# Kernel optimization log

Measured on AMD Instinct MI355X. Metric: run time of the kernel, lower is better.

Reference implementation:

```python
import jax, jax.numpy as jnp
import numpy as np

# ---- module constants (from init_kwargs) ----
EMBED_DIM = 384
NUM_HYPEREDGES = 128
TOPK = 64
SPATIAL_SHAPE = (16, 32, 32)  # D, H, W -> N = 16384
SPACING = (2.0, 1.0, 1.0)
SPATIAL_WEIGHT = 0.1
B, N, C = 4, 16 * 32 * 32, EMBED_DIM


def _l2norm(x, axis=-1, eps=1e-12):
    n = jnp.linalg.norm(x, axis=axis, keepdims=True)
    return x / jnp.maximum(n, eps)


def _get_3d_coords():
    D, H, W = SPATIAL_SHAPE
    z = jnp.arange(D, dtype=jnp.float32) * SPACING[0]
    y = jnp.arange(H, dtype=jnp.float32) * SPACING[1]
    x = jnp.arange(W, dtype=jnp.float32) * SPACING[2]
    zz, yy, xx = jnp.meshgrid(z, y, x, indexing='ij')
    return jnp.stack([zz, yy, xx], axis=-1).reshape(-1, 3)  # (N, 3)


def setup_inputs() -> dict:
    key = jax.random.key(0)
    k1, k2 = jax.random.split(key)
    node_features = jax.random.normal(k1, (B, N, C), dtype=jnp.float32)
    class_token = jax.random.normal(k2, (1, 1, C), dtype=jnp.float32)
    temperature = jnp.ones((1,), dtype=jnp.float32) * 0.07
    return {"node_features": node_features, "class_token": class_token, "temperature": temperature}


def reference(node_features, class_token, temperature):
    Ne = NUM_HYPEREDGES
    w = SPATIAL_WEIGHT
    temp = temperature[0]

    nodes_n = _l2norm(node_features)                      # (B, N, C)

    # Step 1: center sampling by semantic similarity to class token
    ct_n = _l2norm(jnp.broadcast_to(class_token, (B, 1, C)))
    scores = jnp.einsum('boc,bnc->bn', ct_n, nodes_n) / temp  # (B, N)
    _, center_idx = jax.lax.top_k(scores, Ne)             # (B, Ne)

    # Gather centers and compute cosine sim of every center vs all nodes
    centers = jnp.take_along_axis(node_features, center_idx[:, :, None], axis=1)  # (B, Ne, C)
    centers_n = _l2norm(centers)
    sem_sim = jnp.einsum('bec,bnc->ben', centers_n, nodes_n) / temp  # (B, Ne, N)

    # Spatial bias (normalized distance from each center voxel)
    coords = _get_3d_coords()                             # (N, 3)
    center_coords = coords[center_idx]                    # (B, Ne, 3)
    diff = coords[None, None, :, :] - center_coords[:, :, None, :]  # (B, Ne, N, 3)
    dist = jnp.linalg.norm(diff, axis=-1)                 # (B, Ne, N)
    dist = dist / (jnp.max(dist, axis=-1, keepdims=True) + 1e-8)
    combined = (1.0 - w) * sem_sim + w * (1.0 - dist)     # (B, Ne, N)

    # Per-hyperedge top-K neighbors -> incidence matrix H (B, N, Ne)
    _, nbr_idx = jax.lax.top_k(combined, TOPK)            # (B, Ne, K)
    b_ix = jnp.arange(B)[:, None, None]
    e_ix = jnp.arange(Ne)[None, :, None]
    Hmat = jnp.zeros((B, N, Ne), dtype=node_features.dtype)
    Hmat = Hmat.at[b_ix, nbr_idx, e_ix].set(1.0)
    return Hmat
```

## Files before the change

kernel.cpp:

```cpp
#include <hip/hip_runtime.h>
#include <math.h>

#define BB 4
#define NN 16384
#define CC 384
#define NE 128
#define KK 64
#define EQCAP 256

typedef unsigned short ushort_t;
typedef __attribute__((ext_vector_type(8))) short bf16x8;
typedef __attribute__((ext_vector_type(4))) float f32x4;
#define MFMA(a, b, c) __builtin_amdgcn_mfma_f32_16x16x32_bf16(a, b, c, 0, 0, 0)

__device__ inline unsigned fkey(float f) {
    unsigned b = __float_as_uint(f);
    return (b & 0x80000000u) ? ~b : (b | 0x80000000u);
}
__device__ inline ushort_t bf16rne(float f) {
    unsigned u = __float_as_uint(f);
    unsigned r = u + 0x7FFFu + ((u >> 16) & 1u);
    return (ushort_t)(r >> 16);
}
__device__ inline float bf16tof(ushort_t h) {
    return __uint_as_float(((unsigned)h) << 16);
}
__device__ inline void cvt2(float fa, float fb, unsigned& hp, unsigned& lp) {
    unsigned ua = __float_as_uint(fa), ub = __float_as_uint(fb);
    unsigned ra = ua + 0x8000u, rb = ub + 0x8000u;
    hp = (ra >> 16) | (rb & 0xFFFF0000u);
    float ha = __uint_as_float(ra & 0xFFFF0000u);
    float hb = __uint_as_float(rb & 0xFFFF0000u);
    float la = fa - ha, lb = fb - hb;
    unsigned lra = __float_as_uint(la) + 0x8000u;
    unsigned lrb = __float_as_uint(lb) + 0x8000u;
    lp = (lra >> 16) | (lrb & 0xFFFF0000u);
}
__device__ inline void gload16(const void* g, void* l) {
    __builtin_amdgcn_global_load_lds(
        (const __attribute__((address_space(1))) void*)g,
        (__attribute__((address_space(3))) void*)l, 16, 0, 0);
}

__device__ inline void bin_select(unsigned* hist, int t, int* wsum,
                                  int* sh_bin, int* sh_r, int r) {
    int lane = t & 63, wid = t >> 6;
    int c = (t < 256) ? (int)hist[t] : 0;
    int x = c;
#pragma unroll
    for (int off = 1; off < 64; off <<= 1) {
        int v = __shfl_down(x, off, 64);
        if (lane + off < 64) x += v;
    }
    if (lane == 0 && wid < 4) wsum[wid] = x;
    __syncthreads();
    if (t < 256) {
        int add = 0;
        for (int w2 = wid + 1; w2 < 4; ++w2) add += wsum[w2];
        int S_incl = x + add;
        int S_excl = S_incl - c;
        if (S_excl < r && S_incl >= r) { *sh_bin = t; *sh_r = r - S_excl; }
    }
    __syncthreads();
}

__global__ __launch_bounds__(256) void k_scores(const float* __restrict__ nf,
                                                const float* __restrict__ ct,
                                                unsigned* __restrict__ keys,
                                                float* __restrict__ invn) {
    int wave = threadIdx.x >> 6;
    int lane = threadIdx.x & 63;
    int row  = blockIdx.x * 4 + wave;
    const float* x = nf + (size_t)row * CC;
    float4 a  = ((const float4*)x)[lane];
    float2 c2 = ((const float2*)(x + 256))[lane];
    float4 ta = ((const float4*)ct)[lane];
    float2 tc = ((const float2*)(ct + 256))[lane];
    float ss = a.x*a.x + a.y*a.y + a.z*a.z + a.w*a.w + c2.x*c2.x + c2.y*c2.y;
    float dt = ta.x*a.x + ta.y*a.y + ta.z*a.z + ta.w*a.w + tc.x*c2.x + tc.y*c2.y;
#pragma unroll
    for (int off = 32; off; off >>= 1) {
        ss += __shfl_xor(ss, off, 64);
        dt += __shfl_xor(dt, off, 64);
    }
    if (lane == 0) {
        float inv = 1.0f / fmaxf(sqrtf(ss), 1e-12f);
        invn[row] = inv;
        keys[row] = fkey(dt * inv);
    }
}

__global__ __launch_bounds__(1024) void k_top128(const unsigned* __restrict__ keys,
                                                 const float* __restrict__ nf,
                                                 const float* __restrict__ invn,
                                                 ushort_t* __restrict__ Ahi,
                                                 ushort_t* __restrict__ Alo,
                                                 float* __restrict__ meta) {
    __shared__ unsigned hist[256];
    __shared__ int wsum[4];
    __shared__ int sh_bin, sh_r;
    __shared__ unsigned cu[NE];
    __shared__ int cil[NE];
    __shared__ int eqi[EQCAP];
    __shared__ int cnt_gt, cnt_eq;
    __shared__ int ocid[NE];
    int b = blockIdx.x;
    int t = threadIdx.x;
    const uint4* rowv = (const uint4*)(keys + b * NN);
    if (t == 0) { cnt_gt = 0; cnt_eq = 0; }
    unsigned prefix = 0;
    int r = NE;
#pragma unroll
    for (int pass = 0; pass < 4; ++pass) {
        int shift = 24 - 8 * pass;
        unsigned hm = (pass == 0) ? 0u : (0xFFFFFFFFu << (shift + 8));
        if (t < 256) hist[t] = 0;
        __syncthreads();
#pragma unroll
        for (int i = 0; i < 4; ++i) {
            uint4 u = rowv[t + 1024 * i];
            if ((u.x & hm) == (prefix & hm)) atomicAdd(&hist[(u.x >> shift) & 255], 1u);
            if ((u.y & hm) == (prefix & hm)) atomicAdd(&hist[(u.y >> shift) & 255], 1u);
            if ((u.z & hm) == (prefix & hm)) atomicAdd(&hist[(u.z >> shift) & 255], 1u);
            if ((u.w & hm) == (prefix & hm)) atomicAdd(&hist[(u.w >> shift) & 255], 1u);
        }
        __syncthreads();
        bin_select(hist, t, wsum, &sh_bin, &sh_r, r);
        prefix |= ((unsigned)sh_bin) << shift;
        r = sh_r;
        __syncthreads();
    }
    unsigned T = prefix;
#pragma unroll
    for (int i = 0; i < 4; ++i) {
        uint4 u = rowv[t + 1024 * i];
        int nb = 4 * (t + 1024 * i);
        unsigned vv[4] = {u.x, u.y, u.z, u.w};
#pragma unroll
        for (int cmp = 0; cmp < 4; ++cmp) {
            if (vv[cmp] > T) {
                int p = atomicAdd(&cnt_gt, 1);
                cu[p] = vv[cmp]; cil[p] = nb + cmp;
            } else if (vv[cmp] == T) {
                int p = atomicAdd(&cnt_eq, 1);
                if (p < EQCAP) eqi[p] = nb + cmp;
            }
        }
    }
    __syncthreads();
    int ne = cnt_eq < EQCAP ? cnt_eq : EQCAP;
    if (t < ne) {
        int mine = eqi[t], rk = 0;
        for (int j = 0; j < ne; ++j) rk += (eqi[j] < mine);
        if (rk < r) { int p = cnt_gt + rk; cu[p] = T; cil[p] = mine; }
    }
    __syncthreads();
    if (t < NE) {
        unsigned mu = cu[t]; int mi = cil[t], rk = 0;
#pragma unroll 4
        for (int j = 0; j < NE; ++j) {
            unsigned ou = cu[j]; int oi = cil[j];
            rk += (ou > mu) || (ou == mu && oi < mi);
        }
        ocid[rk] = mi;
    }
    __syncthreads();
    {
        int e = t >> 3, part = t & 7;
        int ci = ocid[e];
        float inv = invn[b * NN + ci];
        const float4* src = (const float4*)(nf + ((size_t)b * NN + ci) * CC) + part * 12;
        ushort_t* dh = Ahi + ((size_t)b * NE + e) * CC + part * 48;
        ushort_t* dl = Alo + ((size_t)b * NE + e) * CC + part * 48;
#pragma unroll
        for (int i = 0; i < 12; ++i) {
            float4 f = src[i];
            f.x *= inv; f.y *= inv; f.z *= inv; f.w *= inv;
            ushort4 h, l;
            h.x = bf16rne(f.x); l.x = bf16rne(f.x - bf16tof(h.x));
            h.y = bf16rne(f.y); l.y = bf16rne(f.y - bf16tof(h.y));
            h.z = bf16rne(f.z); l.z = bf16rne(f.z - bf16tof(h.z));
            h.w = bf16rne(f.w); l.w = bf16rne(f.w - bf16tof(h.w));
            ((ushort4*)dh)[i] = h;
            ((ushort4*)dl)[i] = l;
        }
    }
    if (t < NE) {
        int ci = ocid[t];
        float zc = (float)(ci >> 10) * 2.0f;
        float yc = (float)((ci >> 5) & 31);
        float xc = (float)(ci & 31);
        float mz = fmaxf(zc * zc, (30.f - zc) * (30.f - zc));
        float my = fmaxf(yc * yc, (31.f - yc) * (31.f - yc));
        float mx = fmaxf(xc * xc, (31.f - xc) * (31.f - xc));
        float md = sqrtf(mz + my + mx);
        int be = b * NE + t;
        meta[be * 4 + 0] = zc;
        meta[be * 4 + 1] = yc;
        meta[be * 4 + 2] = xc;
        meta[be * 4 + 3] = 1.0f / (md + 1e-8f);
    }
}

__global__ __launch_bounds__(256, 4) void k_gemm(const float* __restrict__ nf,
                                                 const ushort_t* __restrict__ Ahi,
                                                 const ushort_t* __restrict__ Alo,
                                                 const float* __restrict__ invn,
                                                 const float* __restrict__ meta,
                                                 const float* __restrict__ temp,
                                                 unsigned* __restrict__ outk) {
    __shared__ ushort_t Ah[4096], Al[4096];
    __shared__ ushort_t Bhs[2048], Bls[2048];
    __shared__ float ms[NE * 4];
    __shared__ float invs_s[64];
    int b  = blockIdx.y;
    int n0 = blockIdx.x * 64;
    int t  = threadIdx.x;
    int w = t >> 6, lane = t & 63, quad = lane >> 4, mrow = lane & 15;
    int m0 = (w & 1) * 64, nw0 = (w >> 1) * 32;
    for (int i = t; i < NE * 4; i += 256) ms[i] = meta[b * NE * 4 + i];
    if (t < 64) invs_s[t] = invn[b * NN + n0 + t];
    f32x4 acc[4][2];
#pragma unroll
    for (int i = 0; i < 4; ++i)
#pragma unroll
        for (int j = 0; j < 2; ++j) acc[i][j] = (f32x4)0.f;
    const ushort_t* Abh = Ahi + (size_t)b * NE * CC;
    const ushort_t* Abl = Alo + (size_t)b * NE * CC;
    const float* Bb = nf + ((size_t)b * NN + n0) * CC;
    int bn = t >> 2, bk8 = t & 3;
    const float* bsrc = Bb + (size_t)bn * CC + bk8 * 8;
    ushort_t* bh_dst = &Bhs[(bk8 * 64 + bn) * 8];
    ushort_t* bl_dst = &Bls[(bk8 * 64 + bn) * 8];
    const ushort_t* agh0 = Abh + (size_t)(w * 16 + mrow) * CC + quad * 8;
    const ushort_t* agh1 = Abh + (size_t)((w + 4) * 16 + mrow) * CC + quad * 8;
    const ushort_t* agl0 = Abl + (size_t)(w * 16 + mrow) * CC + quad * 8;
    const ushort_t* agl1 = Abl + (size_t)((w + 4) * 16 + mrow) * CC + quad * 8;
    for (int kt = 0; kt < CC; kt += 32) {
        __syncthreads();
        gload16(agh0 + kt, &Ah[w * 512]);
        gload16(agh1 + kt, &Ah[(w + 4) * 512]);
        gload16(agl0 + kt, &Al[w * 512]);
        gload16(agl1 + kt, &Al[(w + 4) * 512]);
        {
            const float4* bs = (const float4*)(bsrc + kt);
            float4 f0 = bs[0];
            float4 f1 = bs[1];
            uint4 ph, pl;
            cvt2(f0.x, f0.y, ph.x, pl.x);
            cvt2(f0.z, f0.w, ph.y, pl.y);
            cvt2(f1.x, f1.y, ph.z, pl.z);
            cvt2(f1.z, f1.w, ph.w, pl.w);
            *(uint4*)bh_dst = ph;
            *(uint4*)bl_dst = pl;
        }
        __syncthreads();
        bf16x8 afh[4], afl[4], bfh[2], bfl[2];
#pragma unroll
        for (int i = 0; i < 4; ++i) {
            int m = m0 + i * 16 + mrow;
            int off = (m >> 4) * 512 + quad * 128 + (m & 15) * 8;
            afh[i] = *(const bf16x8*)&Ah[off];
            afl[i] = *(const bf16x8*)&Al[off];
        }
#pragma unroll
        for (int j = 0; j < 2; ++j) {
            int n = nw0 + j * 16 + mrow;
            bfh[j] = *(const bf16x8*)&Bhs[(quad * 64 + n) * 8];
            bfl[j] = *(const bf16x8*)&Bls[(quad * 64 + n) * 8];
        }
#pragma unroll
        for (int i = 0; i < 4; ++i)
#pragma unroll
            for (int j = 0; j < 2; ++j) {
                acc[i][j] = MFMA(afh[i], bfh[j], acc[i][j]);
                acc[i][j] = MFMA(afh[i], bfl[j], acc[i][j]);
                acc[i][j] = MFMA(afl[i], bfh[j], acc[i][j]);
            }
    }
    float scale = 0.9f / temp[0];
#pragma unroll
    for (int j = 0; j < 2; ++j) {
        int nloc = nw0 + j * 16 + mrow;
        int n = n0 + nloc;
        float invnn = invs_s[nloc];
        float zf = (float)(n >> 10) * 2.0f;
        float yf = (float)((n >> 5) & 31);
        float xf = (float)(n & 31);
#pragma unroll
        for (int i = 0; i < 4; ++i) {
#pragma unroll
            for (int r = 0; r < 4; ++r) {
                int e = m0 + i * 16 + quad * 4 + r;
                float zc = ms[e * 4 + 0], yc = ms[e * 4 + 1], xc = ms[e * 4 + 2], ivd = ms[e * 4 + 3];
                float dz = zf - zc, dy = yf - yc, dx = xf - xc;
                float dist = sqrtf(dz * dz + dy * dy + dx * dx);
                float v = scale * invnn * acc[i][j][r] + 0.1f * (1.0f - dist * ivd);
                outk[((size_t)(b * NE + e)) * NN + n] = fkey(v);
            }
        }
    }
}

__global__ __launch_bounds__(1024) void k_top64(const unsigned* __restrict__ comb,
                                                int* __restrict__ sel) {
    __shared__ unsigned hist[256];
    __shared__ int wsum[4];
    __shared__ int sh_bin, sh_r;
    __shared__ int eqi[EQCAP];
    __shared__ int cnt_gt, cnt_eq;
    int be = blockIdx.x;
    int t  = threadIdx.x;
    const uint4* rowv = (const uint4*)(comb + (size_t)be * NN);
    if (t == 0) { cnt_gt = 0; cnt_eq = 0; }
    unsigned prefix = 0;
    int r = KK;
#pragma unroll
    for (int pass = 0; pass < 4; ++pass) {
        int shift = 24 - 8 * pass;
        unsigned hm = (pass == 0) ? 0u : (0xFFFFFFFFu << (shift + 8));
        if (t < 256) hist[t] = 0;
        __syncthreads();
#pragma unroll
        for (int i = 0; i < 4; ++i) {
            uint4 u = rowv[t + 1024 * i];
            if ((u.x & hm) == (prefix & hm)) atomicAdd(&hist[(u.x >> shift) & 255], 1u);
            if ((u.y & hm) == (prefix & hm)) atomicAdd(&hist[(u.y >> shift) & 255], 1u);
            if ((u.z & hm) == (prefix & hm)) atomicAdd(&hist[(u.z >> shift) & 255], 1u);
            if ((u.w & hm) == (prefix & hm)) atomicAdd(&hist[(u.w >> shift) & 255], 1u);
        }
        __syncthreads();
        bin_select(hist, t, wsum, &sh_bin, &sh_r, r);
        prefix |= ((unsigned)sh_bin) << shift;
        r = sh_r;
        __syncthreads();
    }
    unsigned T = prefix;
#pragma unroll
    for (int i = 0; i < 4; ++i) {
        uint4 u = rowv[t + 1024 * i];
        int nb = 4 * (t + 1024 * i);
        unsigned vv[4] = {u.x, u.y, u.z, u.w};
#pragma unroll
        for (int cmp = 0; cmp < 4; ++cmp) {
            if (vv[cmp] > T) {
                int p = atomicAdd(&cnt_gt, 1);
                sel[be * KK + p] = nb + cmp;
            } else if (vv[cmp] == T) {
                int p = atomicAdd(&cnt_eq, 1);
                if (p < EQCAP) eqi[p] = nb + cmp;
            }
        }
    }
    __syncthreads();
    int ne = cnt_eq < EQCAP ? cnt_eq : EQCAP;
    if (t < ne) {
        int mine = eqi[t], rk = 0;
        for (int j = 0; j < ne; ++j) rk += (eqi[j] < mine);
        if (rk < r) sel[be * KK + cnt_gt + rk] = mine;
    }
}

__global__ __launch_bounds__(256) void k_scatter(const int* __restrict__ sel,
                                                 float* __restrict__ H) {
    int gid = blockIdx.x * 256 + threadIdx.x;
    int b = gid >> 13;
    int e = (gid >> 6) & 127;
    int n = sel[gid];
    H[((size_t)b * NN + n) * NE + e] = 1.0f;
}

extern "C" void kernel_launch(void* const* d_in, const int* in_sizes, int n_in,
                              void* d_out, int out_size, void* d_ws, size_t ws_size,
                              hipStream_t stream) {
    const float* nf   = (const float*)d_in[0];
    const float* ct   = (const float*)d_in[1];
    const float* temp = (const float*)d_in[2];
    float* out = (float*)d_out;

    unsigned* keys = (unsigned*)d_ws;
    float* invn    = (float*)(keys + BB * NN);
    float* meta    = invn + BB * NN;
    ushort_t* Ahi  = (ushort_t*)(meta + BB * NE * 4);
    ushort_t* Alo  = Ahi + (size_t)BB * NE * CC;
    int* sel       = (int*)(Alo + (size_t)BB * NE * CC);

    k_scores <<<BB * NN / 4, 256, 0, stream>>>(nf, ct, keys, invn);
    k_top128 <<<BB, 1024, 0, stream>>>(keys, nf, invn, Ahi, Alo, meta);
    k_gemm   <<<dim3(NN / 64, BB), 256, 0, stream>>>(nf, Ahi, Alo, invn, meta, temp, (unsigned*)out);
    k_top64  <<<BB * NE, 1024, 0, stream>>>((const unsigned*)out, sel);
    hipMemsetAsync(d_out, 0, (size_t)BB * NN * NE * sizeof(float), stream);
    k_scatter<<<BB * NE * KK / 256, 256, 0, stream>>>(sel, out);
}
```

Measured before the change: 287.2 us.

## Replace 4-pass radix select with single 12-bit pass and retile GEMM

Both top-k kernels drop the four 8-bit radix passes for a single 4096-bin histogram on the top 12 key bits. Candidates in the boundary bin are then ranked exactly by key and index in a quadratic pass with capacity 1024, which cuts the repeated reads of each row and the block barriers between passes. The GEMM kernel changes to 64x128 tiles split over hyperedges, uses register prefetch of the next k-slice instead of direct global-to-LDS loads, and pads the LDS layout. The risk is a correctness gap if more than 1024 keys fall in the boundary bin, plus higher LDS use in the top-k kernels.

```diff
diff --git a/kernel.cpp b/kernel.cpp
--- a/kernel.cpp
+++ b/kernel.cpp
@@ -6,7 +6,7 @@
 #define CC 384
 #define NE 128
 #define KK 64
-#define EQCAP 256
+#define CAP 1024
 
 typedef unsigned short ushort_t;
 typedef __attribute__((ext_vector_type(8))) short bf16x8;
@@ -36,31 +36,31 @@
     unsigned lrb = __float_as_uint(lb) + 0x8000u;
     lp = (lra >> 16) | (lrb & 0xFFFF0000u);
 }
-__device__ inline void gload16(const void* g, void* l) {
-    __builtin_amdgcn_global_load_lds(
-        (const __attribute__((address_space(1))) void*)g,
-        (__attribute__((address_space(3))) void*)l, 16, 0, 0);
-}
-
-__device__ inline void bin_select(unsigned* hist, int t, int* wsum,
-                                  int* sh_bin, int* sh_r, int r) {
+
+__device__ inline void bin_select4k(const unsigned* hist, int t, int* wsum,
+                                    int* sh_bin, int* sh_r, int r) {
+    int base = t * 4;
+    int c0 = hist[base], c1 = hist[base + 1], c2 = hist[base + 2], c3 = hist[base + 3];
+    int csum = c0 + c1 + c2 + c3;
     int lane = t & 63, wid = t >> 6;
-    int c = (t < 256) ? (int)hist[t] : 0;
-    int x = c;
+    int x = csum;
 #pragma unroll
     for (int off = 1; off < 64; off <<= 1) {
         int v = __shfl_down(x, off, 64);
         if (lane + off < 64) x += v;
     }
-    if (lane == 0 && wid < 4) wsum[wid] = x;
-    __syncthreads();
-    if (t < 256) {
-        int add = 0;
-        for (int w2 = wid + 1; w2 < 4; ++w2) add += wsum[w2];
-        int S_incl = x + add;
-        int S_excl = S_incl - c;
-        if (S_excl < r && S_incl >= r) { *sh_bin = t; *sh_r = r - S_excl; }
-    }
+    if (lane == 0) wsum[wid] = x;
+    __syncthreads();
+    int after = 0;
+    for (int w2 = wid + 1; w2 < 16; ++w2) after += wsum[w2];
+    int S = x - csum + after;
+    if (S < r && S + c3 >= r) { *sh_bin = base + 3; *sh_r = r - S; }
+    S += c3;
+    if (S < r && S + c2 >= r) { *sh_bin = base + 2; *sh_r = r - S; }
+    S += c2;
+    if (S < r && S + c1 >= r) { *sh_bin = base + 1; *sh_r = r - S; }
+    S += c1;
+    if (S < r && S + c0 >= r) { *sh_bin = base + 0; *sh_r = r - S; }
     __syncthreads();
 }
 
@@ -96,63 +96,51 @@
                                                  ushort_t* __restrict__ Ahi,
                                                  ushort_t* __restrict__ Alo,
                                                  float* __restrict__ meta) {
-    __shared__ unsigned hist[256];
-    __shared__ int wsum[4];
+    __shared__ unsigned hist[4096];
+    __shared__ int wsum[16];
     __shared__ int sh_bin, sh_r;
     __shared__ unsigned cu[NE];
     __shared__ int cil[NE];
-    __shared__ int eqi[EQCAP];
+    __shared__ unsigned eqk[CAP];
+    __shared__ int eqi[CAP];
     __shared__ int cnt_gt, cnt_eq;
     __shared__ int ocid[NE];
     int b = blockIdx.x;
     int t = threadIdx.x;
     const uint4* rowv = (const uint4*)(keys + b * NN);
     if (t == 0) { cnt_gt = 0; cnt_eq = 0; }
-    unsigned prefix = 0;
-    int r = NE;
-#pragma unroll
-    for (int pass = 0; pass < 4; ++pass) {
-        int shift = 24 - 8 * pass;
-        unsigned hm = (pass == 0) ? 0u : (0xFFFFFFFFu << (shift + 8));
-        if (t < 256) hist[t] = 0;
-        __syncthreads();
-#pragma unroll
-        for (int i = 0; i < 4; ++i) {
-            uint4 u = rowv[t + 1024 * i];
-            if ((u.x & hm) == (prefix & hm)) atomicAdd(&hist[(u.x >> shift) & 255], 1u);
-            if ((u.y & hm) == (prefix & hm)) atomicAdd(&hist[(u.y >> shift) & 255], 1u);
-            if ((u.z & hm) == (prefix & hm)) atomicAdd(&hist[(u.z >> shift) & 255], 1u);
-            if ((u.w & hm) == (prefix & hm)) atomicAdd(&hist[(u.w >> shift) & 255], 1u);
-        }
-        __syncthreads();
-        bin_select(hist, t, wsum, &sh_bin, &sh_r, r);
-        prefix |= ((unsigned)sh_bin) << shift;
-        r = sh_r;
-        __syncthreads();
-    }
-    unsigned T = prefix;
-#pragma unroll
-    for (int i = 0; i < 4; ++i) {
-        uint4 u = rowv[t + 1024 * i];
-        int nb = 4 * (t + 1024 * i);
-        unsigned vv[4] = {u.x, u.y, u.z, u.w};
-#pragma unroll
-        for (int cmp = 0; cmp < 4; ++cmp) {
-            if (vv[cmp] > T) {
-                int p = atomicAdd(&cnt_gt, 1);
-                cu[p] = vv[cmp]; cil[p] = nb + cmp;
-            } else if (vv[cmp] == T) {
-                int p = atomicAdd(&cnt_eq, 1);
-                if (p < EQCAP) eqi[p] = nb + cmp;
-            }
-        }
-    }
-    __syncthreads();
-    int ne = cnt_eq < EQCAP ? cnt_eq : EQCAP;
-    if (t < ne) {
-        int mine = eqi[t], rk = 0;
-        for (int j = 0; j < ne; ++j) rk += (eqi[j] < mine);
-        if (rk < r) { int p = cnt_gt + rk; cu[p] = T; cil[p] = mine; }
+    ((uint4*)hist)[t] = make_uint4(0, 0, 0, 0);
+    __syncthreads();
+    uint4 u0 = rowv[t], u1 = rowv[t + 1024], u2 = rowv[t + 2048], u3 = rowv[t + 3072];
+    atomicAdd(&hist[u0.x >> 20], 1u); atomicAdd(&hist[u0.y >> 20], 1u);
+    atomicAdd(&hist[u0.z >> 20], 1u); atomicAdd(&hist[u0.w >> 20], 1u);
+    atomicAdd(&hist[u1.x >> 20], 1u); atomicAdd(&hist[u1.y >> 20], 1u);
+    atomicAdd(&hist[u1.z >> 20], 1u); atomicAdd(&hist[u1.w >> 20], 1u);
+    atomicAdd(&hist[u2.x >> 20], 1u); atomicAdd(&hist[u2.y >> 20], 1u);
+    atomicAdd(&hist[u2.z >> 20], 1u); atomicAdd(&hist[u2.w >> 20], 1u);
+    atomicAdd(&hist[u3.x >> 20], 1u); atomicAdd(&hist[u3.y >> 20], 1u);
+    atomicAdd(&hist[u3.z >> 20], 1u); atomicAdd(&hist[u3.w >> 20], 1u);
+    __syncthreads();
+    bin_select4k(hist, t, wsum, &sh_bin, &sh_r, NE);
+    unsigned bin = (unsigned)sh_bin;
+    int r = sh_r;
+#define EMIT128(uu, nn) { unsigned tb = (uu) >> 20; \
+    if (tb > bin) { int p = atomicAdd(&cnt_gt, 1); cu[p] = (uu); cil[p] = (nn); } \
+    else if (tb == bin) { int p = atomicAdd(&cnt_eq, 1); if (p < CAP) { eqk[p] = (uu); eqi[p] = (nn); } } }
+    EMIT128(u0.x, 4*t+0); EMIT128(u0.y, 4*t+1); EMIT128(u0.z, 4*t+2); EMIT128(u0.w, 4*t+3);
+    EMIT128(u1.x, 4096+4*t+0); EMIT128(u1.y, 4096+4*t+1); EMIT128(u1.z, 4096+4*t+2); EMIT128(u1.w, 4096+4*t+3);
+    EMIT128(u2.x, 8192+4*t+0); EMIT128(u2.y, 8192+4*t+1); EMIT128(u2.z, 8192+4*t+2); EMIT128(u2.w, 8192+4*t+3);
+    EMIT128(u3.x, 12288+4*t+0); EMIT128(u3.y, 12288+4*t+1); EMIT128(u3.z, 12288+4*t+2); EMIT128(u3.w, 12288+4*t+3);
+#undef EMIT128
+    __syncthreads();
+    int ne = cnt_eq < CAP ? cnt_eq : CAP;
+    for (int i = t; i < ne; i += 1024) {
+        unsigned ki = eqk[i]; int ii = eqi[i], rk = 0;
+        for (int j = 0; j < ne; ++j) {
+            unsigned kj = eqk[j];
+            rk += (kj > ki) || (kj == ki && eqi[j] < ii);
+        }
+        if (rk < r) { cu[cnt_gt + rk] = ki; cil[cnt_gt + rk] = ii; }
     }
     __syncthreads();
     if (t < NE) {
@@ -209,70 +197,82 @@
                                                  const float* __restrict__ meta,
                                                  const float* __restrict__ temp,
                                                  unsigned* __restrict__ outk) {
-    __shared__ ushort_t Ah[4096], Al[4096];
-    __shared__ ushort_t Bhs[2048], Bls[2048];
-    __shared__ float ms[NE * 4];
-    __shared__ float invs_s[64];
+    __shared__ ushort_t Ah[4][66][8], Al[4][66][8];
+    __shared__ ushort_t Bh[4][130][8], Bl[4][130][8];
+    __shared__ float ms[64 * 4];
+    __shared__ float invs_s[128];
     int b  = blockIdx.y;
-    int n0 = blockIdx.x * 64;
+    int e0 = (blockIdx.x & 1) * 64;
+    int n0 = (blockIdx.x >> 1) * 128;
     int t  = threadIdx.x;
     int w = t >> 6, lane = t & 63, quad = lane >> 4, mrow = lane & 15;
-    int m0 = (w & 1) * 64, nw0 = (w >> 1) * 32;
-    for (int i = t; i < NE * 4; i += 256) ms[i] = meta[b * NE * 4 + i];
-    if (t < 64) invs_s[t] = invn[b * NN + n0 + t];
-    f32x4 acc[4][2];
-#pragma unroll
-    for (int i = 0; i < 4; ++i)
-#pragma unroll
-        for (int j = 0; j < 2; ++j) acc[i][j] = (f32x4)0.f;
-    const ushort_t* Abh = Ahi + (size_t)b * NE * CC;
-    const ushort_t* Abl = Alo + (size_t)b * NE * CC;
+    int m0 = (w & 1) * 32, nw0 = (w >> 1) * 64;
+    for (int i = t; i < 64 * 4; i += 256) ms[i] = meta[(b * NE + e0) * 4 + i];
+    if (t < 128) invs_s[t] = invn[b * NN + n0 + t];
+    f32x4 acc[2][4];
+#pragma unroll
+    for (int i = 0; i < 2; ++i)
+#pragma unroll
+        for (int j = 0; j < 4; ++j) acc[i][j] = (f32x4)0.f;
+    const ushort_t* Abh = Ahi + ((size_t)b * NE + e0) * CC;
+    const ushort_t* Abl = Alo + ((size_t)b * NE + e0) * CC;
     const float* Bb = nf + ((size_t)b * NN + n0) * CC;
-    int bn = t >> 2, bk8 = t & 3;
-    const float* bsrc = Bb + (size_t)bn * CC + bk8 * 8;
-    ushort_t* bh_dst = &Bhs[(bk8 * 64 + bn) * 8];
-    ushort_t* bl_dst = &Bls[(bk8 * 64 + bn) * 8];
-    const ushort_t* agh0 = Abh + (size_t)(w * 16 + mrow) * CC + quad * 8;
-    const ushort_t* agh1 = Abh + (size_t)((w + 4) * 16 + mrow) * CC + quad * 8;
-    const ushort_t* agl0 = Abl + (size_t)(w * 16 + mrow) * CC + quad * 8;
-    const ushort_t* agl1 = Abl + (size_t)((w + 4) * 16 + mrow) * CC + quad * 8;
+    int ae = t >> 2, ak8 = t & 3;
+    const ushort_t* agh = Abh + (size_t)ae * CC + ak8 * 8;
+    const ushort_t* agl = Abl + (size_t)ae * CC + ak8 * 8;
+    int bn0 = t >> 2, bk80 = t & 3;
+    int bn1 = (t + 256) >> 2, bk81 = (t + 256) & 3;
+    const float* bs0 = Bb + (size_t)bn0 * CC + bk80 * 8;
+    const float* bs1 = Bb + (size_t)bn1 * CC + bk81 * 8;
+    uint4 pAh, pAl;
+    float4 pB0a, pB0b, pB1a, pB1b;
+    pAh = *(const uint4*)agh;
+    pAl = *(const uint4*)agl;
+    pB0a = ((const float4*)bs0)[0]; pB0b = ((const float4*)bs0)[1];
+    pB1a = ((const float4*)bs1)[0]; pB1b = ((const float4*)bs1)[1];
     for (int kt = 0; kt < CC; kt += 32) {
         __syncthreads();
-        gload16(agh0 + kt, &Ah[w * 512]);
-        gload16(agh1 + kt, &Ah[(w + 4) * 512]);
-        gload16(agl0 + kt, &Al[w * 512]);
-        gload16(agl1 + kt, &Al[(w + 4) * 512]);
+        *(uint4*)&Ah[ak8][ae][0] = pAh;
+        *(uint4*)&Al[ak8][ae][0] = pAl;
         {
-            const float4* bs = (const float4*)(bsrc + kt);
-            float4 f0 = bs[0];
-            float4 f1 = bs[1];
             uint4 ph, pl;
-            cvt2(f0.x, f0.y, ph.x, pl.x);
-            cvt2(f0.z, f0.w, ph.y, pl.y);
-            cvt2(f1.x, f1.y, ph.z, pl.z);
-            cvt2(f1.z, f1.w, ph.w, pl.w);
-            *(uint4*)bh_dst = ph;
-            *(uint4*)bl_dst = pl;
+            cvt2(pB0a.x, pB0a.y, ph.x, pl.x);
+            cvt2(pB0a.z, pB0a.w, ph.y, pl.y);
+            cvt2(pB0b.x, pB0b.y, ph.z, pl.z);
+            cvt2(pB0b.z, pB0b.w, ph.w, pl.w);
+            *(uint4*)&Bh[bk80][bn0][0] = ph;
+            *(uint4*)&Bl[bk80][bn0][0] = pl;
+            cvt2(pB1a.x, pB1a.y, ph.x, pl.x);
+            cvt2(pB1a.z, pB1a.w, ph.y, pl.y);
+            cvt2(pB1b.x, pB1b.y, ph.z, pl.z);
+            cvt2(pB1b.z, pB1b.w, ph.w, pl.w);
+            *(uint4*)&Bh[bk81][bn1][0] = ph;
+            *(uint4*)&Bl[bk81][bn1][0] = pl;
+        }
+        if (kt + 32 < CC) {
+            pAh = *(const uint4*)(agh + kt + 32);
+            pAl = *(const uint4*)(agl + kt + 32);
+            pB0a = ((const float4*)(bs0 + kt + 32))[0]; pB0b = ((const float4*)(bs0 + kt + 32))[1];
+            pB1a = ((const float4*)(bs1 + kt + 32))[0]; pB1b = ((const float4*)(bs1 + kt + 32))[1];
         }
         __syncthreads();
-        bf16x8 afh[4], afl[4], bfh[2], bfl[2];
-#pragma unroll
-        for (int i = 0; i < 4; ++i) {
+        bf16x8 afh[2], afl[2], bfh[4], bfl[4];
+#pragma unroll
+        for (int i = 0; i < 2; ++i) {
             int m = m0 + i * 16 + mrow;
-            int off = (m >> 4) * 512 + quad * 128 + (m & 15) * 8;
-            afh[i] = *(const bf16x8*)&Ah[off];
-            afl[i] = *(const bf16x8*)&Al[off];
-        }
-#pragma unroll
-        for (int j = 0; j < 2; ++j) {
+            afh[i] = *(const bf16x8*)&Ah[quad][m][0];
+            afl[i] = *(const bf16x8*)&Al[quad][m][0];
+        }
+#pragma unroll
+        for (int j = 0; j < 4; ++j) {
             int n = nw0 + j * 16 + mrow;
-            bfh[j] = *(const bf16x8*)&Bhs[(quad * 64 + n) * 8];
-            bfl[j] = *(const bf16x8*)&Bls[(quad * 64 + n) * 8];
-        }
-#pragma unroll
-        for (int i = 0; i < 4; ++i)
-#pragma unroll
-            for (int j = 0; j < 2; ++j) {
+            bfh[j] = *(const bf16x8*)&Bh[quad][n][0];
+            bfl[j] = *(const bf16x8*)&Bl[quad][n][0];
+        }
+#pragma unroll
+        for (int i = 0; i < 2; ++i)
+#pragma unroll
+            for (int j = 0; j < 4; ++j) {
                 acc[i][j] = MFMA(afh[i], bfh[j], acc[i][j]);
                 acc[i][j] = MFMA(afh[i], bfl[j], acc[i][j]);
                 acc[i][j] = MFMA(afl[i], bfh[j], acc[i][j]);
@@ -280,7 +280,7 @@
     }
     float scale = 0.9f / temp[0];
 #pragma unroll
-    for (int j = 0; j < 2; ++j) {
+    for (int j = 0; j < 4; ++j) {
         int nloc = nw0 + j * 16 + mrow;
         int n = n0 + nloc;
         float invnn = invs_s[nloc];
@@ -288,15 +288,15 @@
         float yf = (float)((n >> 5) & 31);
         float xf = (float)(n & 31);
 #pragma unroll
-        for (int i = 0; i < 4; ++i) {
+        for (int i = 0; i < 2; ++i) {
 #pragma unroll
             for (int r = 0; r < 4; ++r) {
-                int e = m0 + i * 16 + quad * 4 + r;
-                float zc = ms[e * 4 + 0], yc = ms[e * 4 + 1], xc = ms[e * 4 + 2], ivd = ms[e * 4 + 3];
+                int el = m0 + i * 16 + quad * 4 + r;
+                float zc = ms[el * 4 + 0], yc = ms[el * 4 + 1], xc = ms[el * 4 + 2], ivd = ms[el * 4 + 3];
                 float dz = zf - zc, dy = yf - yc, dx = xf - xc;
                 float dist = sqrtf(dz * dz + dy * dy + dx * dx);
                 float v = scale * invnn * acc[i][j][r] + 0.1f * (1.0f - dist * ivd);
-                outk[((size_t)(b * NE + e)) * NN + n] = fkey(v);
+                outk[((size_t)(b * NE + e0 + el)) * NN + n] = fkey(v);
             }
         }
     }
@@ -304,60 +304,48 @@
 
 __global__ __launch_bounds__(1024) void k_top64(const unsigned* __restrict__ comb,
                                                 int* __restrict__ sel) {
-    __shared__ unsigned hist[256];
-    __shared__ int wsum[4];
+    __shared__ unsigned hist[4096];
+    __shared__ int wsum[16];
     __shared__ int sh_bin, sh_r;
-    __shared__ int eqi[EQCAP];
+    __shared__ unsigned eqk[CAP];
+    __shared__ int eqi[CAP];
     __shared__ int cnt_gt, cnt_eq;
     int be = blockIdx.x;
     int t  = threadIdx.x;
     const uint4* rowv = (const uint4*)(comb + (size_t)be * NN);
     if (t == 0) { cnt_gt = 0; cnt_eq = 0; }
-    unsigned prefix = 0;
-    int r = KK;
-#pragma unroll
-    for (int pass = 0; pass < 4; ++pass) {
-        int shift = 24 - 8 * pass;
-        unsigned hm = (pass == 0) ? 0u : (0xFFFFFFFFu << (shift + 8));
-        if (t < 256) hist[t] = 0;
-        __syncthreads();
-#pragma unroll
-        for (int i = 0; i < 4; ++i) {
-            uint4 u = rowv[t + 1024 * i];
-            if ((u.x & hm) == (prefix & hm)) atomicAdd(&hist[(u.x >> shift) & 255], 1u);
-            if ((u.y & hm) == (prefix & hm)) atomicAdd(&hist[(u.y >> shift) & 255], 1u);
-            if ((u.z & hm) == (prefix & hm)) atomicAdd(&hist[(u.z >> shift) & 255], 1u);
-            if ((u.w & hm) == (prefix & hm)) atomicAdd(&hist[(u.w >> shift) & 255], 1u);
-        }
-        __syncthreads();
-        bin_select(hist, t, wsum, &sh_bin, &sh_r, r);
-        prefix |= ((unsigned)sh_bin) << shift;
-        r = sh_r;
-        __syncthreads();
-    }
-    unsigned T = prefix;
-#pragma unroll
-    for (int i = 0; i < 4; ++i) {
-        uint4 u = rowv[t + 1024 * i];
-        int nb = 4 * (t + 1024 * i);
-        unsigned vv[4] = {u.x, u.y, u.z, u.w};
-#pragma unroll
-        for (int cmp = 0; cmp < 4; ++cmp) {
-            if (vv[cmp] > T) {
-                int p = atomicAdd(&cnt_gt, 1);
-                sel[be * KK + p] = nb + cmp;
-            } else if (vv[cmp] == T) {
-                int p = atomicAdd(&cnt_eq, 1);
-                if (p < EQCAP) eqi[p] = nb + cmp;
-            }
-        }
-    }
-    __syncthreads();
-    int ne = cnt_eq < EQCAP ? cnt_eq : EQCAP;
-    if (t < ne) {
-        int mine = eqi[t], rk = 0;
-        for (int j = 0; j < ne; ++j) rk += (eqi[j] < mine);
-        if (rk < r) sel[be * KK + cnt_gt + rk] = mine;
+    ((uint4*)hist)[t] = make_uint4(0, 0, 0, 0);
+    __syncthreads();
+    uint4 u0 = rowv[t], u1 = rowv[t + 1024], u2 = rowv[t + 2048], u3 = rowv[t + 3072];
+    atomicAdd(&hist[u0.x >> 20], 1u); atomicAdd(&hist[u0.y >> 20], 1u);
+    atomicAdd(&hist[u0.z >> 20], 1u); atomicAdd(&hist[u0.w >> 20], 1u);
+    atomicAdd(&hist[u1.x >> 20], 1u); atomicAdd(&hist[u1.y >> 20], 1u);
+    atomicAdd(&hist[u1.z >> 20], 1u); atomicAdd(&hist[u1.w >> 20], 1u);
+    atomicAdd(&hist[u2.x >> 20], 1u); atomicAdd(&hist[u2.y >> 20], 1u);
+    atomicAdd(&hist[u2.z >> 20], 1u); atomicAdd(&hist[u2.w >> 20], 1u);
+    atomicAdd(&hist[u3.x >> 20], 1u); atomicAdd(&hist[u3.y >> 20], 1u);
+    atomicAdd(&hist[u3.z >> 20], 1u); atomicAdd(&hist[u3.w >> 20], 1u);
+    __syncthreads();
+    bin_select4k(hist, t, wsum, &sh_bin, &sh_r, KK);
+    unsigned bin = (unsigned)sh_bin;
+    int r = sh_r;
+#define EMIT64(uu, nn) { unsigned tb = (uu) >> 20; \
+    if (tb > bin) { int p = atomicAdd(&cnt_gt, 1); sel[be * KK + p] = (nn); } \
+    else if (tb == bin) { int p = atomicAdd(&cnt_eq, 1); if (p < CAP) { eqk[p] = (uu); eqi[p] = (nn); } } }
+    EMIT64(u0.x, 4*t+0); EMIT64(u0.y, 4*t+1); EMIT64(u0.z, 4*t+2); EMIT64(u0.w, 4*t+3);
+    EMIT64(u1.x, 4096+4*t+0); EMIT64(u1.y, 4096+4*t+1); EMIT64(u1.z, 4096+4*t+2); EMIT64(u1.w, 4096+4*t+3);
+    EMIT64(u2.x, 8192+4*t+0); EMIT64(u2.y, 8192+4*t+1); EMIT64(u2.z, 8192+4*t+2); EMIT64(u2.w, 8192+4*t+3);
+    EMIT64(u3.x, 12288+4*t+0); EMIT64(u3.y, 12288+4*t+1); EMIT64(u3.z, 12288+4*t+2); EMIT64(u3.w, 12288+4*t+3);
+#undef EMIT64
+    __syncthreads();
+    int ne = cnt_eq < CAP ? cnt_eq : CAP;
+    for (int i = t; i < ne; i += 1024) {
+        unsigned ki = eqk[i]; int ii = eqi[i], rk = 0;
+        for (int j = 0; j < ne; ++j) {
+            unsigned kj = eqk[j];
+            rk += (kj > ki) || (kj == ki && eqi[j] < ii);
+        }
+        if (rk < r) sel[be * KK + cnt_gt + rk] = ii;
     }
 }
 
@@ -387,7 +375,7 @@
 
     k_scores <<<BB * NN / 4, 256, 0, stream>>>(nf, ct, keys, invn);
     k_top128 <<<BB, 1024, 0, stream>>>(keys, nf, invn, Ahi, Alo, meta);
-    k_gemm   <<<dim3(NN / 64, BB), 256, 0, stream>>>(nf, Ahi, Alo, invn, meta, temp, (unsigned*)out);
+    k_gemm   <<<dim3(NN / 128 * 2, BB), 256, 0, stream>>>(nf, Ahi, Alo, invn, meta, temp, (unsigned*)out);
     k_top64  <<<BB * NE, 1024, 0, stream>>>((const unsigned*)out, sel);
     hipMemsetAsync(d_out, 0, (size_t)BB * NN * NE * sizeof(float), stream);
     k_scatter<<<BB * NE * KK / 256, 256, 0, stream>>>(sel, out);
```

Result: faster. 254.4 us (-11.4%).
